# Kernel tuning notes

Measured on AMD Instinct MI355X. Metric: run time of the kernel, lower is better.

Reference implementation:

```python
import jax, jax.numpy as jnp
import numpy as np

N = 50000   # nodes
E = 600000  # edges per relation
F = 256     # dim_features
H = 128     # dim_hiddens == dim_embs
Q = 64      # dim_query
R = 2       # relations per sign (etypes)
L = 2       # conv_depth


def setup_inputs() -> dict:
    key = jax.random.key(0)
    ks = jax.random.split(key, 11)
    s = 0.05
    return {
        "x_attr": jax.random.normal(ks[0], (N, F), jnp.float32),
        "x_stru": jax.random.normal(ks[1], (N, F), jnp.float32),
        # edges_*: [sign(pos/neg), relation, (src,dst), E]
        "edges_attr": jax.random.randint(ks[2], (2, R, 2, E), 0, N),
        "edges_stru": jax.random.randint(ks[3], (2, R, 2, E), 0, N),
        # params, leading dim 2 = (pos_emb_model, neg_emb_model)
        "Wf": jax.random.normal(ks[4], (2, H, F), jnp.float32) * s,
        "convW": jax.random.normal(ks[5], (2, L, R, H, H), jnp.float32) * s,
        "convB": jnp.zeros((2, L, R, H), jnp.float32),
        "attnW1": jax.random.normal(ks[6], (2, L, H, Q), jnp.float32) * s,
        "attnB1": jnp.zeros((2, L, Q), jnp.float32),
        "attnW2": jax.random.normal(ks[7], (2, L, Q), jnp.float32) * s,
        "Wc": jax.random.normal(ks[8], (2, H, 3 * H), jnp.float32) * s,
    }


def _gcn(h, src, dst, W, b):
    """DGL GraphConv, norm='both', degrees clamped to >=1."""
    n = h.shape[0]
    ones = jnp.ones(src.shape[0], h.dtype)
    deg_out = jnp.clip(jax.ops.segment_sum(ones, src, num_segments=n), 1.0)
    deg_in = jnp.clip(jax.ops.segment_sum(ones, dst, num_segments=n), 1.0)
    m = (h * (deg_out ** -0.5)[:, None]) @ W          # (N, H)
    agg = jax.ops.segment_sum(m[src], dst, num_segments=n)  # gather-scatter over edges
    return agg * (deg_in ** -0.5)[:, None] + b


def _het_layer(h, edges, Ws, bs, W1, b1, w2):
    """HeteroGraphConv with per-node attention aggregation over relations.
    edges: (R, 2, E); Ws: (R,H,H); bs: (R,H)."""
    hs = jnp.stack([_gcn(h, edges[r, 0], edges[r, 1], Ws[r], bs[r]) for r in range(R)])  # (R,N,H)
    scores = jnp.einsum('rnq,q->rn', jnp.tanh(jnp.einsum('rnd,dq->rnq', hs, W1) + b1), w2)
    a = jax.nn.softmax(scores, axis=0)                # (R,N) attention over relations
    return jnp.einsum('rn,rnd->nd', a, hs), a


def _hetattn(x, edges, Wf, cW, cB, aW1, aB1, aW2, Wc):
    h0 = jnp.tanh(x @ Wf.T)                                        # (N,H)
    h1, _ = _het_layer(h0, edges, cW[1], cB[1], aW1[1], aB1[1], aW2[1])   # 1-hop via last conv
    hA, _ = _het_layer(h0, edges, cW[0], cB[0], aW1[0], aB1[0], aW2[0])
    h2, attn = _het_layer(hA, edges, cW[1], cB[1], aW1[1], aB1[1], aW2[1])  # 2-hop
    y = jnp.concatenate([h0, h1, h2], axis=-1) @ Wc.T              # concat_weight
    return y, attn.T


def reference(x_attr, x_stru, edges_attr, edges_stru, Wf, convW, convB,
              attnW1, attnB1, attnW2, Wc):
    def run(sign, x, edges):
        y, _ = _hetattn(x, edges[sign], Wf[sign], convW[sign], convB[sign],
                        attnW1[sign], attnB1[sign], attnW2[sign], Wc[sign])
        return y
    embs_attr_pos = run(0, x_attr, edges_attr)
    embs_stru_pos = run(0, x_stru, edges_stru)
    embs_attr_neg = run(1, x_attr, edges_attr)
    embs_stru_neg = run(1, x_stru, edges_stru)
    return (embs_attr_pos, embs_stru_pos, embs_attr_neg, embs_stru_neg)
```

## Files before the change

### kernel.cpp

```cpp
#include <hip/hip_runtime.h>
#include <math.h>

constexpr int N_ = 50000;
constexpr int E_ = 600000;
constexpr int F_ = 256;
constexpr int H_ = 128;
constexpr int Q_ = 64;
constexpr int R_ = 2;
constexpr int L_ = 2;

#define MODE_STORE 0
#define MODE_TANH  1
#define MODE_ACC   2

template <bool BT>
__global__ __launch_bounds__(256) void gemm_kernel(
    const float* __restrict__ A, int lda,
    const float* __restrict__ B, int ldb,
    float* __restrict__ C, int ldc,
    int M, int K,
    const float* __restrict__ rowscale, int mode)
{
    __shared__ __align__(16) float As[2][16][68];
    __shared__ __align__(16) float Bs[2][16][132];

    const int row0 = blockIdx.x * 64;
    const int col0 = blockIdx.y * 128;
    const int tid  = threadIdx.x;
    const int tm = tid >> 4;
    const int tn = tid & 15;

    const int am  = tid >> 2;
    const int ak4 = (tid & 3) * 4;
    const int bj  = tid >> 1;
    const int bk8 = (tid & 1) * 8;
    const int bk  = tid >> 5;
    const int bj4 = (tid & 31) * 4;

    auto loadA = [&](int kk) -> float4 {
        const int r = row0 + am;
        if (r < M) return *(const float4*)(A + (size_t)r * lda + kk + ak4);
        return make_float4(0.f, 0.f, 0.f, 0.f);
    };
    auto loadB = [&](int kk, float4& v0, float4& v1) {
        if (BT) {
            const float* bp = B + (size_t)(col0 + bj) * ldb + kk + bk8;
            v0 = *(const float4*)(bp);
            v1 = *(const float4*)(bp + 4);
        } else {
            v0 = *(const float4*)(B + (size_t)(kk + bk) * ldb + col0 + bj4);
            v1 = *(const float4*)(B + (size_t)(kk + bk + 8) * ldb + col0 + bj4);
        }
    };
    auto storeT = [&](int b, float4 va, float4 v0, float4 v1) {
        As[b][ak4 + 0][am] = va.x; As[b][ak4 + 1][am] = va.y;
        As[b][ak4 + 2][am] = va.z; As[b][ak4 + 3][am] = va.w;
        if (BT) {
            Bs[b][bk8 + 0][bj] = v0.x; Bs[b][bk8 + 1][bj] = v0.y;
            Bs[b][bk8 + 2][bj] = v0.z; Bs[b][bk8 + 3][bj] = v0.w;
            Bs[b][bk8 + 4][bj] = v1.x; Bs[b][bk8 + 5][bj] = v1.y;
            Bs[b][bk8 + 6][bj] = v1.z; Bs[b][bk8 + 7][bj] = v1.w;
        } else {
            Bs[b][bk + 0][bj4 + 0] = v0.x; Bs[b][bk + 0][bj4 + 1] = v0.y;
            Bs[b][bk + 0][bj4 + 2] = v0.z; Bs[b][bk + 0][bj4 + 3] = v0.w;
            Bs[b][bk + 8][bj4 + 0] = v1.x; Bs[b][bk + 8][bj4 + 1] = v1.y;
            Bs[b][bk + 8][bj4 + 2] = v1.z; Bs[b][bk + 8][bj4 + 3] = v1.w;
        }
    };

    float acc[4][8] = {};

    {
        float4 va = loadA(0), v0, v1;
        loadB(0, v0, v1);
        storeT(0, va, v0, v1);
    }
    __syncthreads();

    int cur = 0;
    for (int kk = 16; ; kk += 16) {
        const bool more = (kk < K);
        float4 na, n0, n1;
        if (more) { na = loadA(kk); loadB(kk, n0, n1); }

        #pragma unroll
        for (int k = 0; k < 16; k++) {
            const float4 av  = *(const float4*)&As[cur][k][tm * 4];
            const float4 bv0 = *(const float4*)&Bs[cur][k][tn * 8];
            const float4 bv1 = *(const float4*)&Bs[cur][k][tn * 8 + 4];
            const float a[4] = {av.x, av.y, av.z, av.w};
            const float b[8] = {bv0.x, bv0.y, bv0.z, bv0.w,
                                bv1.x, bv1.y, bv1.z, bv1.w};
            #pragma unroll
            for (int i = 0; i < 4; i++)
                #pragma unroll
                for (int j = 0; j < 8; j++)
                    acc[i][j] += a[i] * b[j];
        }
        if (!more) break;
        storeT(cur ^ 1, na, n0, n1);
        __syncthreads();
        cur ^= 1;
    }

    #pragma unroll
    for (int i = 0; i < 4; i++) {
        const int r = row0 + tm * 4 + i;
        if (r >= M) continue;
        const float rs = rowscale ? rowscale[r] : 1.0f;
        #pragma unroll
        for (int j = 0; j < 8; j++) {
            const int c = col0 + tn * 8 + j;
            float v = acc[i][j] * rs;
            if (mode == MODE_TANH) v = tanhf(v);
            float* p = C + (size_t)r * ldc + c;
            if (mode == MODE_ACC) *p += v;
            else                  *p = v;
        }
    }
}

__global__ __launch_bounds__(256) void gemm_conv_pair(
    const float* __restrict__ A, int lda,
    const float* __restrict__ B0, const float* __restrict__ B1,
    float* __restrict__ C0, float* __restrict__ C1,
    int M, const float* __restrict__ rs0, const float* __restrict__ rs1)
{
    __shared__ __align__(16) float As[2][16][68];
    __shared__ __align__(16) float B0s[2][16][68];
    __shared__ __align__(16) float B1s[2][16][68];

    const int row0 = blockIdx.x * 64;
    const int col0 = blockIdx.y * 64;
    const int tid  = threadIdx.x;
    const int tm = tid >> 4;
    const int tn = tid & 15;

    const int am  = tid >> 2;
    const int ak4 = (tid & 3) * 4;
    const int bk  = tid >> 4;
    const int bj4 = (tid & 15) * 4;

    auto loadA = [&](int kk) -> float4 {
        const int r = row0 + am;
        if (r < M) return *(const float4*)(A + (size_t)r * lda + kk + ak4);
        return make_float4(0.f, 0.f, 0.f, 0.f);
    };
    auto storeT = [&](int b, float4 va, float4 v0, float4 v1) {
        As[b][ak4 + 0][am] = va.x; As[b][ak4 + 1][am] = va.y;
        As[b][ak4 + 2][am] = va.z; As[b][ak4 + 3][am] = va.w;
        B0s[b][bk][bj4 + 0] = v0.x; B0s[b][bk][bj4 + 1] = v0.y;
        B0s[b][bk][bj4 + 2] = v0.z; B0s[b][bk][bj4 + 3] = v0.w;
        B1s[b][bk][bj4 + 0] = v1.x; B1s[b][bk][bj4 + 1] = v1.y;
        B1s[b][bk][bj4 + 2] = v1.z; B1s[b][bk][bj4 + 3] = v1.w;
    };

    float acc0[4][4] = {};
    float acc1[4][4] = {};

    {
        float4 va = loadA(0);
        float4 v0 = *(const float4*)(B0 + (size_t)bk * H_ + col0 + bj4);
        float4 v1 = *(const float4*)(B1 + (size_t)bk * H_ + col0 + bj4);
        storeT(0, va, v0, v1);
    }
    __syncthreads();

    int cur = 0;
    for (int kk = 16; ; kk += 16) {
        const bool more = (kk < H_);
        float4 na, n0, n1;
        if (more) {
            na = loadA(kk);
            n0 = *(const float4*)(B0 + (size_t)(kk + bk) * H_ + col0 + bj4);
            n1 = *(const float4*)(B1 + (size_t)(kk + bk) * H_ + col0 + bj4);
        }

        #pragma unroll
        for (int k = 0; k < 16; k++) {
            const float4 av  = *(const float4*)&As[cur][k][tm * 4];
            const float4 bv0 = *(const float4*)&B0s[cur][k][tn * 4];
            const float4 bv1 = *(const float4*)&B1s[cur][k][tn * 4];
            const float a[4]  = {av.x, av.y, av.z, av.w};
            const float b0[4] = {bv0.x, bv0.y, bv0.z, bv0.w};
            const float b1v[4] = {bv1.x, bv1.y, bv1.z, bv1.w};
            #pragma unroll
            for (int i = 0; i < 4; i++)
                #pragma unroll
                for (int j = 0; j < 4; j++) {
                    acc0[i][j] += a[i] * b0[j];
                    acc1[i][j] += a[i] * b1v[j];
                }
        }
        if (!more) break;
        storeT(cur ^ 1, na, n0, n1);
        __syncthreads();
        cur ^= 1;
    }

    #pragma unroll
    for (int i = 0; i < 4; i++) {
        const int r = row0 + tm * 4 + i;
        if (r >= M) continue;
        const float s0 = rs0[r];
        const float s1 = rs1[r];
        #pragma unroll
        for (int j = 0; j < 4; j++) {
            const int c = col0 + tn * 4 + j;
            C0[(size_t)r * H_ + c] = acc0[i][j] * s0;
            C1[(size_t)r * H_ + c] = acc1[i][j] * s1;
        }
    }
}

__global__ __launch_bounds__(256) void zero_i(int* __restrict__ p, int n)
{
    int t = blockIdx.x * 256 + threadIdx.x;
    if (t < n) p[t] = 0;
}

__global__ __launch_bounds__(256) void count_deg(const int* __restrict__ eb,
                                                 int* __restrict__ cnt, int total)
{
    int t = blockIdx.x * 256 + threadIdx.x;
    if (t >= total) return;
    int which = t / E_;
    atomicAdd(&cnt[which * N_ + eb[t]], 1);
}

__global__ __launch_bounds__(256) void deg_finalize(const int* __restrict__ cnt,
                                                    float* __restrict__ dscale, int n)
{
    int t = blockIdx.x * 256 + threadIdx.x;
    if (t < n) {
        int v = cnt[t];
        dscale[t] = rsqrtf((float)(v < 1 ? 1 : v));
    }
}

constexpr int SCAN_NB = (N_ + 255) / 256;

__global__ __launch_bounds__(256) void scan_p1(const int* __restrict__ cnt,
                                               int* __restrict__ bsums)
{
    const int r = blockIdx.y;
    const int* in = cnt + (size_t)(2 * r + 1) * N_;
    const int i = blockIdx.x * 256 + threadIdx.x;
    int v = (i < N_) ? in[i] : 0;
    #pragma unroll
    for (int off = 32; off > 0; off >>= 1) v += __shfl_xor(v, off);
    __shared__ int ws[4];
    if ((threadIdx.x & 63) == 0) ws[threadIdx.x >> 6] = v;
    __syncthreads();
    if (threadIdx.x == 0)
        bsums[r * SCAN_NB + blockIdx.x] = ws[0] + ws[1] + ws[2] + ws[3];
}

__global__ __launch_bounds__(256) void scan_p2(int* __restrict__ bsums)
{
    __shared__ int sh[256];
    const int r = blockIdx.x;
    const int t = threadIdx.x;
    int v = (t < SCAN_NB) ? bsums[r * SCAN_NB + t] : 0;
    sh[t] = v;
    __syncthreads();
    #pragma unroll
    for (int d = 1; d < 256; d <<= 1) {
        int u = (t >= d) ? sh[t - d] : 0;
        __syncthreads();
        sh[t] += u;
        __syncthreads();
    }
    if (t < SCAN_NB) bsums[r * SCAN_NB + t] = sh[t] - v;
}

__global__ __launch_bounds__(256) void scan_p3(const int* __restrict__ cnt,
                                               const int* __restrict__ bsums,
                                               int* __restrict__ offs,
                                               int* __restrict__ cursor)
{
    __shared__ int sh[256];
    const int r = blockIdx.y;
    const int* in = cnt + (size_t)(2 * r + 1) * N_;
    int* out = offs + (size_t)r * (N_ + 1);
    int* cur = cursor + (size_t)r * N_;
    const int i = blockIdx.x * 256 + threadIdx.x;
    const int t = threadIdx.x;
    int v = (i < N_) ? in[i] : 0;
    sh[t] = v;
    __syncthreads();
    #pragma unroll
    for (int d = 1; d < 256; d <<= 1) {
        int u = (t >= d) ? sh[t - d] : 0;
        __syncthreads();
        sh[t] += u;
        __syncthreads();
    }
    const int excl = sh[t] - v + bsums[r * SCAN_NB + blockIdx.x];
    if (i < N_) { out[i] = excl; cur[i] = excl; }
    if (i == 0) out[N_] = E_;
}

__global__ __launch_bounds__(256) void csr_fill(const int* __restrict__ eb,
                                                int* __restrict__ cursor,
                                                int* __restrict__ csr, int total)
{
    int t = blockIdx.x * 256 + threadIdx.x;
    if (t >= total) return;
    int r = (t >= E_) ? 1 : 0;
    int e = t - r * E_;
    int s = eb[(r * 2 + 0) * E_ + e];
    int d = eb[(r * 2 + 1) * E_ + e];
    int pos = atomicAdd(&cursor[r * N_ + d], 1);
    csr[(size_t)r * E_ + pos] = s;
}

__device__ __forceinline__ void gather_rel(const float2* __restrict__ m,
                                           const int* __restrict__ csr,
                                           int b, int e, int lane, float2& acc)
{
    int k = b;
    for (; k + 4 <= e; k += 4) {
        const int s0 = csr[k + 0];
        const int s1 = csr[k + 1];
        const int s2 = csr[k + 2];
        const int s3 = csr[k + 3];
        const float2 v0 = m[(size_t)s0 * 64 + lane];
        const float2 v1 = m[(size_t)s1 * 64 + lane];
        const float2 v2 = m[(size_t)s2 * 64 + lane];
        const float2 v3 = m[(size_t)s3 * 64 + lane];
        acc.x += (v0.x + v1.x) + (v2.x + v3.x);
        acc.y += (v0.y + v1.y) + (v2.y + v3.y);
    }
    for (; k < e; k++) {
        const int s = csr[k];
        const float2 v = m[(size_t)s * 64 + lane];
        acc.x += v.x; acc.y += v.y;
    }
}

__global__ __launch_bounds__(1024, 8) void pull_attn(
    const float2* __restrict__ m0, const float2* __restrict__ m1,
    const int* __restrict__ offs0, const int* __restrict__ csr0,
    const int* __restrict__ offs1, const int* __restrict__ csr1,
    const float* __restrict__ si0, const float* __restrict__ si1,
    const float* __restrict__ bias0, const float* __restrict__ bias1,
    const float* __restrict__ W1, const float* __restrict__ b1,
    const float* __restrict__ w2, float2* __restrict__ outb, int n)
{
    __shared__ float W1s[H_ * Q_];
    __shared__ __align__(16) float2 hsS[16][2][Q_];
    __shared__ float b1s[Q_], w2s[Q_], bAs[H_], bBs[H_];

    for (int i = threadIdx.x; i < H_ * Q_; i += 1024) W1s[i] = W1[i];
    if (threadIdx.x < Q_) { b1s[threadIdx.x] = b1[threadIdx.x]; w2s[threadIdx.x] = w2[threadIdx.x]; }
    {
        const int t = (int)threadIdx.x - Q_;
        if (t >= 0 && t < H_) bAs[t] = bias0[t];
        const int u = (int)threadIdx.x - Q_ - H_;
        if (u >= 0 && u < H_) bBs[u] = bias1[u];
    }
    __syncthreads();

    const int lane = threadIdx.x & 63;
    const int wv   = threadIdx.x >> 6;
    int node = (blockIdx.x * 1024 + threadIdx.x) >> 6;
    node = __builtin_amdgcn_readfirstlane(node);

    float2 hs0 = make_float2(0.f, 0.f), hs1 = hs0;

    if (node < n) {
        float2 a0 = make_float2(0.f, 0.f), a1 = a0;
        const int b0  = offs0[node], e0 = offs0[node + 1];
        const int b1i = offs1[node], e1 = offs1[node + 1];
        gather_rel(m0, csr0, b0,  e0, lane, a0);
        gather_rel(m1, csr1, b1i, e1, lane, a1);

        const float sc0 = si0[node], sc1 = si1[node];
        hs0.x = a0.x * sc0 + bAs[2 * lane];
        hs0.y = a0.y * sc0 + bAs[2 * lane + 1];
        hs1.x = a1.x * sc1 + bBs[2 * lane];
        hs1.y = a1.y * sc1 + bBs[2 * lane + 1];
        hsS[wv][0][lane] = hs0;
        hsS[wv][1][lane] = hs1;
    }

    __asm__ volatile("s_waitcnt lgkmcnt(0)" ::: "memory");
    __builtin_amdgcn_sched_barrier(0);

    if (node < n) {
        const float4* h0p4 = (const float4*)&hsS[wv][0][0];
        const float4* h1p4 = (const float4*)&hsS[wv][1][0];
        float t0 = b1s[lane], t1 = b1s[lane];
        #pragma unroll 8
        for (int i4 = 0; i4 < 32; i4++) {
            const float4 h0v = h0p4[i4];
            const float4 h1v = h1p4[i4];
            const float wa = W1s[(i4 * 4 + 0) * Q_ + lane];
            const float wb = W1s[(i4 * 4 + 1) * Q_ + lane];
            const float wc = W1s[(i4 * 4 + 2) * Q_ + lane];
            const float wd = W1s[(i4 * 4 + 3) * Q_ + lane];
            t0 += h0v.x * wa + h0v.y * wb + h0v.z * wc + h0v.w * wd;
            t1 += h1v.x * wa + h1v.y * wb + h1v.z * wc + h1v.w * wd;
        }
        float s0 = tanhf(t0) * w2s[lane];
        float s1 = tanhf(t1) * w2s[lane];
        #pragma unroll
        for (int off = 32; off > 0; off >>= 1) {
            s0 += __shfl_xor(s0, off);
            s1 += __shfl_xor(s1, off);
        }
        const float mx = fmaxf(s0, s1);
        const float e0v = expf(s0 - mx), e1v = expf(s1 - mx);
        const float a0 = e0v / (e0v + e1v), a1 = 1.0f - a0;

        float2 o;
        o.x = a0 * hs0.x + a1 * hs1.x;
        o.y = a0 * hs0.y + a1 * hs1.y;
        outb[(size_t)node * 64 + lane] = o;
    }
}

extern "C" void kernel_launch(void* const* d_in, const int* in_sizes, int n_in,
                              void* d_out, int out_size, void* d_ws, size_t ws_size,
                              hipStream_t stream)
{
    const float* x_attr = (const float*)d_in[0];
    const float* x_stru = (const float*)d_in[1];
    const int*   e_attr = (const int*)d_in[2];
    const int*   e_stru = (const int*)d_in[3];
    const float* Wf     = (const float*)d_in[4];
    const float* convW  = (const float*)d_in[5];
    const float* convB  = (const float*)d_in[6];
    const float* aW1    = (const float*)d_in[7];
    const float* aB1    = (const float*)d_in[8];
    const float* aW2    = (const float*)d_in[9];
    const float* Wc     = (const float*)d_in[10];
    float*       out    = (float*)d_out;
    float*       ws     = (float*)d_ws;

    const size_t NH = (size_t)N_ * H_;
    float* A  = ws;
    float* Bb = ws + 1 * NH;
    float* C  = ws + 2 * NH;
    float* D  = ws + 3 * NH;
    float* dscale = ws + 4 * NH;
    int*   ibase  = (int*)(dscale + 4 * N_);
    int*   cnt    = ibase;
    int*   offs   = ibase + 4 * N_;
    int*   csr    = offs + 2 * (N_ + 1);
    int*   cursor = csr + 2 * E_;
    int*   bsums  = cursor + 2 * N_;

    const int GX = (N_ + 63) / 64;
    const dim3 GGEMM(GX, 1);
    const dim3 GCONV(GX, 2);
    const dim3 GSCAN(SCAN_NB, 2);
    const int PA_B = (N_ * 64) / 1024;

    for (int run = 0; run < 4; run++) {
        const int sign = run >> 1;
        const float* x = (run & 1) ? x_stru : x_attr;
        const int* eb = ((run & 1) ? e_stru : e_attr) + (size_t)sign * (R_ * 2 * E_);
        float* y = out + (size_t)run * NH;
        const float* WcS = Wc + (size_t)sign * H_ * 3 * H_;

        zero_i<<<(4 * N_ + 255) / 256, 256, 0, stream>>>(cnt, 4 * N_);
        count_deg<<<(4 * E_ + 255) / 256, 256, 0, stream>>>(eb, cnt, 4 * E_);
        deg_finalize<<<(4 * N_ + 255) / 256, 256, 0, stream>>>(cnt, dscale, 4 * N_);
        scan_p1<<<GSCAN, 256, 0, stream>>>(cnt, bsums);
        scan_p2<<<2, 256, 0, stream>>>(bsums);
        scan_p3<<<GSCAN, 256, 0, stream>>>(cnt, bsums, offs, cursor);
        csr_fill<<<(2 * E_ + 255) / 256, 256, 0, stream>>>(eb, cursor, csr, 2 * E_);

        gemm_kernel<true><<<GGEMM, 256, 0, stream>>>(
            x, F_, Wf + (size_t)sign * H_ * F_, F_, A, H_, N_, F_, nullptr, MODE_TANH);

        gemm_kernel<true><<<GGEMM, 256, 0, stream>>>(
            A, H_, WcS, 3 * H_, y, H_, N_, H_, nullptr, MODE_STORE);

        auto het = [&](const float* h_in, int l, float* outb) {
            const size_t lo = (size_t)(sign * L_ + l);
            gemm_conv_pair<<<GCONV, 256, 0, stream>>>(
                h_in, H_,
                convW + (lo * R_ + 0) * H_ * H_,
                convW + (lo * R_ + 1) * H_ * H_,
                C, D, N_,
                dscale + 0 * N_, dscale + 2 * N_);
            pull_attn<<<PA_B, 1024, 0, stream>>>(
                (const float2*)C, (const float2*)D,
                offs, csr, offs + (N_ + 1), csr + E_,
                dscale + N_, dscale + 3 * N_,
                convB + (lo * R_ + 0) * H_, convB + (lo * R_ + 1) * H_,
                aW1 + lo * H_ * Q_, aB1 + lo * Q_, aW2 + lo * Q_,
                (float2*)outb, N_);
        };

        het(A, 1, Bb);
        gemm_kernel<true><<<GGEMM, 256, 0, stream>>>(
            Bb, H_, WcS + H_, 3 * H_, y, H_, N_, H_, nullptr, MODE_ACC);

        het(A, 0, Bb);

        het(Bb, 1, A);
        gemm_kernel<true><<<GGEMM, 256, 0, stream>>>(
            A, H_, WcS + 2 * H_, 3 * H_, y, H_, N_, H_, nullptr, MODE_ACC);
    }
}
```

Baseline: 3.467 ms.

## Aggregate before transform, share first-hop gather, fold attention projection into conv GEMM

Each layer now gathers neighbours first and then applies the GEMM, instead of transforming first and then gathering. The per-edge source-degree scale is stored alongside the CSR during construction. Because the 1-hop pass and layer 0 both aggregate h0, they share one gather, so each run does two gathers instead of three. The attention projection W·W1 and its bias are precomputed once, so the conv GEMM emits both the hidden output and the attention pre-activations, and a light kernel applies tanh, softmax and the combine. The cost is an extra buffer for the scores, per-edge scale reads in the gather, and a wider GEMM tile.

```diff
diff --git a/kernel.cpp b/kernel.cpp
--- a/kernel.cpp
+++ b/kernel.cpp
@@ -120,96 +120,142 @@
     }
 }
 
-__global__ __launch_bounds__(256) void gemm_conv_pair(
-    const float* __restrict__ A, int lda,
-    const float* __restrict__ B0, const float* __restrict__ B1,
-    float* __restrict__ C0, float* __restrict__ C1,
-    int M, const float* __restrict__ rs0, const float* __restrict__ rs1)
+__global__ __launch_bounds__(256) void conv_dual(
+    const float* g0, const float* g1,
+    const float* __restrict__ Wlo,
+    const float* __restrict__ WWlo,
+    float* hs0, float* hs1,
+    float* T,
+    int M)
 {
     __shared__ __align__(16) float As[2][16][68];
-    __shared__ __align__(16) float B0s[2][16][68];
-    __shared__ __align__(16) float B1s[2][16][68];
+    __shared__ __align__(16) float Bs[2][16][200];
+
+    const int r = blockIdx.y;
+    const float* A  = r ? g1 : g0;
+    const float* __restrict__ W  = Wlo  + (size_t)r * H_ * H_;
+    const float* __restrict__ WW = WWlo + (size_t)r * H_ * Q_;
+    float* hs = r ? hs1 : hs0;
+    float* Tr = T + (size_t)r * M * Q_;
 
     const int row0 = blockIdx.x * 64;
-    const int col0 = blockIdx.y * 64;
     const int tid  = threadIdx.x;
     const int tm = tid >> 4;
     const int tn = tid & 15;
 
     const int am  = tid >> 2;
     const int ak4 = (tid & 3) * 4;
-    const int bk  = tid >> 4;
-    const int bj4 = (tid & 15) * 4;
+
+    int bk_[3], bc_[3];
+    #pragma unroll
+    for (int i = 0; i < 3; i++) {
+        const int f = tid + i * 256;
+        bk_[i] = f / 48;
+        bc_[i] = (f % 48) * 4;
+    }
 
     auto loadA = [&](int kk) -> float4 {
-        const int r = row0 + am;
-        if (r < M) return *(const float4*)(A + (size_t)r * lda + kk + ak4);
+        const int rr = row0 + am;
+        if (rr < M) return *(const float4*)(A + (size_t)rr * H_ + kk + ak4);
         return make_float4(0.f, 0.f, 0.f, 0.f);
     };
-    auto storeT = [&](int b, float4 va, float4 v0, float4 v1) {
+    auto loadB = [&](int kk, float4* v) {
+        #pragma unroll
+        for (int i = 0; i < 3; i++) {
+            const int k = kk + bk_[i];
+            const int c = bc_[i];
+            v[i] = (c < H_) ? *(const float4*)(W  + (size_t)k * H_ + c)
+                            : *(const float4*)(WW + (size_t)k * Q_ + (c - H_));
+        }
+    };
+    auto storeT = [&](int b, float4 va, const float4* v) {
         As[b][ak4 + 0][am] = va.x; As[b][ak4 + 1][am] = va.y;
         As[b][ak4 + 2][am] = va.z; As[b][ak4 + 3][am] = va.w;
-        B0s[b][bk][bj4 + 0] = v0.x; B0s[b][bk][bj4 + 1] = v0.y;
-        B0s[b][bk][bj4 + 2] = v0.z; B0s[b][bk][bj4 + 3] = v0.w;
-        B1s[b][bk][bj4 + 0] = v1.x; B1s[b][bk][bj4 + 1] = v1.y;
-        B1s[b][bk][bj4 + 2] = v1.z; B1s[b][bk][bj4 + 3] = v1.w;
+        #pragma unroll
+        for (int i = 0; i < 3; i++) {
+            Bs[b][bk_[i]][bc_[i] + 0] = v[i].x;
+            Bs[b][bk_[i]][bc_[i] + 1] = v[i].y;
+            Bs[b][bk_[i]][bc_[i] + 2] = v[i].z;
+            Bs[b][bk_[i]][bc_[i] + 3] = v[i].w;
+        }
     };
 
-    float acc0[4][4] = {};
-    float acc1[4][4] = {};
+    float acc[4][12] = {};
 
     {
-        float4 va = loadA(0);
-        float4 v0 = *(const float4*)(B0 + (size_t)bk * H_ + col0 + bj4);
-        float4 v1 = *(const float4*)(B1 + (size_t)bk * H_ + col0 + bj4);
-        storeT(0, va, v0, v1);
+        float4 va = loadA(0), vb[3];
+        loadB(0, vb);
+        storeT(0, va, vb);
     }
     __syncthreads();
 
     int cur = 0;
     for (int kk = 16; ; kk += 16) {
         const bool more = (kk < H_);
-        float4 na, n0, n1;
-        if (more) {
-            na = loadA(kk);
-            n0 = *(const float4*)(B0 + (size_t)(kk + bk) * H_ + col0 + bj4);
-            n1 = *(const float4*)(B1 + (size_t)(kk + bk) * H_ + col0 + bj4);
-        }
+        float4 na, nb[3];
+        if (more) { na = loadA(kk); loadB(kk, nb); }
 
         #pragma unroll
         for (int k = 0; k < 16; k++) {
             const float4 av  = *(const float4*)&As[cur][k][tm * 4];
-            const float4 bv0 = *(const float4*)&B0s[cur][k][tn * 4];
-            const float4 bv1 = *(const float4*)&B1s[cur][k][tn * 4];
+            const float4 bv0 = *(const float4*)&Bs[cur][k][tn * 12];
+            const float4 bv1 = *(const float4*)&Bs[cur][k][tn * 12 + 4];
+            const float4 bv2 = *(const float4*)&Bs[cur][k][tn * 12 + 8];
             const float a[4]  = {av.x, av.y, av.z, av.w};
-            const float b0[4] = {bv0.x, bv0.y, bv0.z, bv0.w};
-            const float b1v[4] = {bv1.x, bv1.y, bv1.z, bv1.w};
+            const float b[12] = {bv0.x, bv0.y, bv0.z, bv0.w,
+                                 bv1.x, bv1.y, bv1.z, bv1.w,
+                                 bv2.x, bv2.y, bv2.z, bv2.w};
             #pragma unroll
             for (int i = 0; i < 4; i++)
                 #pragma unroll
-                for (int j = 0; j < 4; j++) {
-                    acc0[i][j] += a[i] * b0[j];
-                    acc1[i][j] += a[i] * b1v[j];
-                }
+                for (int j = 0; j < 12; j++)
+                    acc[i][j] += a[i] * b[j];
         }
         if (!more) break;
-        storeT(cur ^ 1, na, n0, n1);
+        storeT(cur ^ 1, na, nb);
         __syncthreads();
         cur ^= 1;
     }
 
     #pragma unroll
     for (int i = 0; i < 4; i++) {
-        const int r = row0 + tm * 4 + i;
-        if (r >= M) continue;
-        const float s0 = rs0[r];
-        const float s1 = rs1[r];
+        const int rr = row0 + tm * 4 + i;
+        if (rr >= M) continue;
         #pragma unroll
-        for (int j = 0; j < 4; j++) {
-            const int c = col0 + tn * 4 + j;
-            C0[(size_t)r * H_ + c] = acc0[i][j] * s0;
-            C1[(size_t)r * H_ + c] = acc1[i][j] * s1;
-        }
+        for (int j = 0; j < 12; j++) {
+            const int c = tn * 12 + j;
+            const float v = acc[i][j];
+            if (c < H_) hs[(size_t)rr * H_ + c] = v;
+            else        Tr[(size_t)rr * Q_ + (c - H_)] = v;
+        }
+    }
+}
+
+__global__ __launch_bounds__(256) void prep_ww1(
+    const float* __restrict__ convW, const float* __restrict__ convB,
+    const float* __restrict__ aW1, const float* __restrict__ aB1,
+    float* __restrict__ ww1, float* __restrict__ bbq)
+{
+    const int c  = blockIdx.x;
+    const int lo = c >> 1;
+    const int r  = c & 1;
+    const float* W  = convW + ((size_t)lo * R_ + r) * H_ * H_;
+    const float* W1 = aW1 + (size_t)lo * H_ * Q_;
+    const float* bs = convB + ((size_t)lo * R_ + r) * H_;
+    const float* b1 = aB1 + (size_t)lo * Q_;
+    float* o = ww1 + (size_t)c * H_ * Q_;
+
+    for (int ofs = threadIdx.x; ofs < H_ * Q_; ofs += 256) {
+        const int k = ofs >> 6, q = ofs & 63;
+        float s = 0.f;
+        for (int i = 0; i < H_; i++) s += W[k * H_ + i] * W1[i * Q_ + q];
+        o[ofs] = s;
+    }
+    if (threadIdx.x < Q_) {
+        const int q = threadIdx.x;
+        float s = 0.f;
+        for (int i = 0; i < H_; i++) s += bs[i] * W1[i * Q_ + q];
+        bbq[c * Q_ + q] = s + b1[q];
     }
 }
 
@@ -303,7 +349,9 @@
 
 __global__ __launch_bounds__(256) void csr_fill(const int* __restrict__ eb,
                                                 int* __restrict__ cursor,
-                                                int* __restrict__ csr, int total)
+                                                int* __restrict__ csr,
+                                                const float* __restrict__ dscale,
+                                                float* __restrict__ scl, int total)
 {
     int t = blockIdx.x * 256 + threadIdx.x;
     if (t >= total) return;
@@ -313,112 +361,112 @@
     int d = eb[(r * 2 + 1) * E_ + e];
     int pos = atomicAdd(&cursor[r * N_ + d], 1);
     csr[(size_t)r * E_ + pos] = s;
-}
-
-__device__ __forceinline__ void gather_rel(const float2* __restrict__ m,
-                                           const int* __restrict__ csr,
-                                           int b, int e, int lane, float2& acc)
-{
-    int k = b;
-    for (; k + 4 <= e; k += 4) {
-        const int s0 = csr[k + 0];
-        const int s1 = csr[k + 1];
-        const int s2 = csr[k + 2];
-        const int s3 = csr[k + 3];
-        const float2 v0 = m[(size_t)s0 * 64 + lane];
-        const float2 v1 = m[(size_t)s1 * 64 + lane];
-        const float2 v2 = m[(size_t)s2 * 64 + lane];
-        const float2 v3 = m[(size_t)s3 * 64 + lane];
-        acc.x += (v0.x + v1.x) + (v2.x + v3.x);
-        acc.y += (v0.y + v1.y) + (v2.y + v3.y);
-    }
-    for (; k < e; k++) {
-        const int s = csr[k];
-        const float2 v = m[(size_t)s * 64 + lane];
-        acc.x += v.x; acc.y += v.y;
-    }
-}
-
-__global__ __launch_bounds__(1024, 8) void pull_attn(
-    const float2* __restrict__ m0, const float2* __restrict__ m1,
-    const int* __restrict__ offs0, const int* __restrict__ csr0,
-    const int* __restrict__ offs1, const int* __restrict__ csr1,
+    scl[(size_t)r * E_ + pos] = dscale[(size_t)(2 * r) * N_ + s];
+}
+
+__global__ __launch_bounds__(256) void gather2(
+    const float2* __restrict__ h,
+    const int* __restrict__ offs0, const int* __restrict__ csr0, const float* __restrict__ scl0,
+    const int* __restrict__ offs1, const int* __restrict__ csr1, const float* __restrict__ scl1,
+    float2* __restrict__ g0, float2* __restrict__ g1, int n)
+{
+    const int lane = threadIdx.x & 63;
+    int node = (blockIdx.x * 256 + threadIdx.x) >> 6;
+    node = __builtin_amdgcn_readfirstlane(node);
+    if (node >= n) return;
+
+    float2 a0 = make_float2(0.f, 0.f), a1 = a0;
+    {
+        int k = offs0[node];
+        const int e = offs0[node + 1];
+        for (; k + 4 <= e; k += 4) {
+            const int s0 = csr0[k + 0], s1 = csr0[k + 1];
+            const int s2 = csr0[k + 2], s3 = csr0[k + 3];
+            const float w0 = scl0[k + 0], w1 = scl0[k + 1];
+            const float w2v = scl0[k + 2], w3 = scl0[k + 3];
+            const float2 v0 = h[(size_t)s0 * 64 + lane];
+            const float2 v1 = h[(size_t)s1 * 64 + lane];
+            const float2 v2 = h[(size_t)s2 * 64 + lane];
+            const float2 v3 = h[(size_t)s3 * 64 + lane];
+            a0.x += v0.x * w0 + v1.x * w1 + v2.x * w2v + v3.x * w3;
+            a0.y += v0.y * w0 + v1.y * w1 + v2.y * w2v + v3.y * w3;
+        }
+        for (; k < e; k++) {
+            const int s = csr0[k];
+            const float w = scl0[k];
+            const float2 v = h[(size_t)s * 64 + lane];
+            a0.x += v.x * w; a0.y += v.y * w;
+        }
+    }
+    {
+        int k = offs1[node];
+        const int e = offs1[node + 1];
+        for (; k + 4 <= e; k += 4) {
+            const int s0 = csr1[k + 0], s1 = csr1[k + 1];
+            const int s2 = csr1[k + 2], s3 = csr1[k + 3];
+            const float w0 = scl1[k + 0], w1 = scl1[k + 1];
+            const float w2v = scl1[k + 2], w3 = scl1[k + 3];
+            const float2 v0 = h[(size_t)s0 * 64 + lane];
+            const float2 v1 = h[(size_t)s1 * 64 + lane];
+            const float2 v2 = h[(size_t)s2 * 64 + lane];
+            const float2 v3 = h[(size_t)s3 * 64 + lane];
+            a1.x += v0.x * w0 + v1.x * w1 + v2.x * w2v + v3.x * w3;
+            a1.y += v0.y * w0 + v1.y * w1 + v2.y * w2v + v3.y * w3;
+        }
+        for (; k < e; k++) {
+            const int s = csr1[k];
+            const float w = scl1[k];
+            const float2 v = h[(size_t)s * 64 + lane];
+            a1.x += v.x * w; a1.y += v.y * w;
+        }
+    }
+    g0[(size_t)node * 64 + lane] = a0;
+    g1[(size_t)node * 64 + lane] = a1;
+}
+
+__global__ __launch_bounds__(256) void attn_comb(
+    const float2* hs0p, const float2* hs1p,
+    const float* __restrict__ T0, const float* __restrict__ T1,
     const float* __restrict__ si0, const float* __restrict__ si1,
     const float* __restrict__ bias0, const float* __restrict__ bias1,
-    const float* __restrict__ W1, const float* __restrict__ b1,
-    const float* __restrict__ w2, float2* __restrict__ outb, int n)
-{
-    __shared__ float W1s[H_ * Q_];
-    __shared__ __align__(16) float2 hsS[16][2][Q_];
-    __shared__ float b1s[Q_], w2s[Q_], bAs[H_], bBs[H_];
-
-    for (int i = threadIdx.x; i < H_ * Q_; i += 1024) W1s[i] = W1[i];
-    if (threadIdx.x < Q_) { b1s[threadIdx.x] = b1[threadIdx.x]; w2s[threadIdx.x] = w2[threadIdx.x]; }
-    {
-        const int t = (int)threadIdx.x - Q_;
-        if (t >= 0 && t < H_) bAs[t] = bias0[t];
-        const int u = (int)threadIdx.x - Q_ - H_;
-        if (u >= 0 && u < H_) bBs[u] = bias1[u];
-    }
+    const float* __restrict__ bbq0, const float* __restrict__ bbq1,
+    const float* __restrict__ w2,
+    float2* outb, int n)
+{
+    __shared__ float bbqA[Q_], bbqB[Q_], w2s[Q_], bAs[H_], bBs[H_];
+    const int tid = threadIdx.x;
+    if (tid < Q_) { bbqA[tid] = bbq0[tid]; w2s[tid] = w2[tid]; }
+    else if (tid < 2 * Q_) bbqB[tid - Q_] = bbq1[tid - Q_];
+    if (tid < H_) bAs[tid] = bias0[tid];
+    else bBs[tid - H_] = bias1[tid - H_];
     __syncthreads();
 
-    const int lane = threadIdx.x & 63;
-    const int wv   = threadIdx.x >> 6;
-    int node = (blockIdx.x * 1024 + threadIdx.x) >> 6;
+    const int lane = tid & 63;
+    int node = (blockIdx.x * 256 + tid) >> 6;
     node = __builtin_amdgcn_readfirstlane(node);
-
-    float2 hs0 = make_float2(0.f, 0.f), hs1 = hs0;
-
-    if (node < n) {
-        float2 a0 = make_float2(0.f, 0.f), a1 = a0;
-        const int b0  = offs0[node], e0 = offs0[node + 1];
-        const int b1i = offs1[node], e1 = offs1[node + 1];
-        gather_rel(m0, csr0, b0,  e0, lane, a0);
-        gather_rel(m1, csr1, b1i, e1, lane, a1);
-
-        const float sc0 = si0[node], sc1 = si1[node];
-        hs0.x = a0.x * sc0 + bAs[2 * lane];
-        hs0.y = a0.y * sc0 + bAs[2 * lane + 1];
-        hs1.x = a1.x * sc1 + bBs[2 * lane];
-        hs1.y = a1.y * sc1 + bBs[2 * lane + 1];
-        hsS[wv][0][lane] = hs0;
-        hsS[wv][1][lane] = hs1;
-    }
-
-    __asm__ volatile("s_waitcnt lgkmcnt(0)" ::: "memory");
-    __builtin_amdgcn_sched_barrier(0);
-
-    if (node < n) {
-        const float4* h0p4 = (const float4*)&hsS[wv][0][0];
-        const float4* h1p4 = (const float4*)&hsS[wv][1][0];
-        float t0 = b1s[lane], t1 = b1s[lane];
-        #pragma unroll 8
-        for (int i4 = 0; i4 < 32; i4++) {
-            const float4 h0v = h0p4[i4];
-            const float4 h1v = h1p4[i4];
-            const float wa = W1s[(i4 * 4 + 0) * Q_ + lane];
-            const float wb = W1s[(i4 * 4 + 1) * Q_ + lane];
-            const float wc = W1s[(i4 * 4 + 2) * Q_ + lane];
-            const float wd = W1s[(i4 * 4 + 3) * Q_ + lane];
-            t0 += h0v.x * wa + h0v.y * wb + h0v.z * wc + h0v.w * wd;
-            t1 += h1v.x * wa + h1v.y * wb + h1v.z * wc + h1v.w * wd;
-        }
-        float s0 = tanhf(t0) * w2s[lane];
-        float s1 = tanhf(t1) * w2s[lane];
-        #pragma unroll
-        for (int off = 32; off > 0; off >>= 1) {
-            s0 += __shfl_xor(s0, off);
-            s1 += __shfl_xor(s1, off);
-        }
-        const float mx = fmaxf(s0, s1);
-        const float e0v = expf(s0 - mx), e1v = expf(s1 - mx);
-        const float a0 = e0v / (e0v + e1v), a1 = 1.0f - a0;
-
-        float2 o;
-        o.x = a0 * hs0.x + a1 * hs1.x;
-        o.y = a0 * hs0.y + a1 * hs1.y;
-        outb[(size_t)node * 64 + lane] = o;
-    }
+    if (node >= n) return;
+
+    const float t0v = T0[(size_t)node * Q_ + lane];
+    const float t1v = T1[(size_t)node * Q_ + lane];
+    const float si0n = si0[node], si1n = si1[node];
+    const float2 h0v = hs0p[(size_t)node * 64 + lane];
+    const float2 h1v = hs1p[(size_t)node * 64 + lane];
+
+    float s0 = tanhf(si0n * t0v + bbqA[lane]) * w2s[lane];
+    float s1 = tanhf(si1n * t1v + bbqB[lane]) * w2s[lane];
+    #pragma unroll
+    for (int off = 32; off > 0; off >>= 1) {
+        s0 += __shfl_xor(s0, off);
+        s1 += __shfl_xor(s1, off);
+    }
+    const float mx = fmaxf(s0, s1);
+    const float e0v = expf(s0 - mx), e1v = expf(s1 - mx);
+    const float a0 = e0v / (e0v + e1v), a1 = 1.0f - a0;
+
+    float2 o;
+    o.x = a0 * (h0v.x * si0n + bAs[2 * lane])     + a1 * (h1v.x * si1n + bBs[2 * lane]);
+    o.y = a0 * (h0v.y * si0n + bAs[2 * lane + 1]) + a1 * (h1v.y * si1n + bBs[2 * lane + 1]);
+    outb[(size_t)node * 64 + lane] = o;
 }
 
 extern "C" void kernel_launch(void* const* d_in, const int* in_sizes, int n_in,
@@ -444,19 +492,26 @@
     float* Bb = ws + 1 * NH;
     float* C  = ws + 2 * NH;
     float* D  = ws + 3 * NH;
-    float* dscale = ws + 4 * NH;
+    float* Tb = ws + 4 * NH;
+    float* dscale = ws + 5 * NH;
     int*   ibase  = (int*)(dscale + 4 * N_);
     int*   cnt    = ibase;
-    int*   offs   = ibase + 4 * N_;
-    int*   csr    = offs + 2 * (N_ + 1);
+    int*   offs   = cnt + 4 * N_;
+    constexpr int OFFS_PAD = 2 * (N_ + 1) + 2;
+    int*   csr    = offs + OFFS_PAD;
     int*   cursor = csr + 2 * E_;
     int*   bsums  = cursor + 2 * N_;
+    float* scl    = (float*)(bsums + 2 * SCAN_NB);
+    float* ww1    = scl + 2 * (size_t)E_;
+    float* bbq    = ww1 + 8 * H_ * Q_;
 
     const int GX = (N_ + 63) / 64;
     const dim3 GGEMM(GX, 1);
     const dim3 GCONV(GX, 2);
     const dim3 GSCAN(SCAN_NB, 2);
-    const int PA_B = (N_ * 64) / 1024;
+    const int PW_B = (N_ * 64) / 256;
+
+    prep_ww1<<<8, 256, 0, stream>>>(convW, convB, aW1, aB1, ww1, bbq);
 
     for (int run = 0; run < 4; run++) {
         const int sign = run >> 1;
@@ -471,7 +526,8 @@
         scan_p1<<<GSCAN, 256, 0, stream>>>(cnt, bsums);
         scan_p2<<<2, 256, 0, stream>>>(bsums);
         scan_p3<<<GSCAN, 256, 0, stream>>>(cnt, bsums, offs, cursor);
-        csr_fill<<<(2 * E_ + 255) / 256, 256, 0, stream>>>(eb, cursor, csr, 2 * E_);
+        csr_fill<<<(2 * E_ + 255) / 256, 256, 0, stream>>>(eb, cursor, csr,
+                                                           dscale, scl, 2 * E_);
 
         gemm_kernel<true><<<GGEMM, 256, 0, stream>>>(
             x, F_, Wf + (size_t)sign * H_ * F_, F_, A, H_, N_, F_, nullptr, MODE_TANH);
@@ -479,31 +535,39 @@
         gemm_kernel<true><<<GGEMM, 256, 0, stream>>>(
             A, H_, WcS, 3 * H_, y, H_, N_, H_, nullptr, MODE_STORE);
 
-        auto het = [&](const float* h_in, int l, float* outb) {
+        gather2<<<PW_B, 256, 0, stream>>>(
+            (const float2*)A, offs, csr, scl, offs + (N_ + 1), csr + E_, scl + E_,
+            (float2*)C, (float2*)D, N_);
+
+        auto convattn = [&](int l, float* hsA, float* hsB, float* dest) {
             const size_t lo = (size_t)(sign * L_ + l);
-            gemm_conv_pair<<<GCONV, 256, 0, stream>>>(
-                h_in, H_,
-                convW + (lo * R_ + 0) * H_ * H_,
-                convW + (lo * R_ + 1) * H_ * H_,
-                C, D, N_,
-                dscale + 0 * N_, dscale + 2 * N_);
-            pull_attn<<<PA_B, 1024, 0, stream>>>(
-                (const float2*)C, (const float2*)D,
-                offs, csr, offs + (N_ + 1), csr + E_,
+            conv_dual<<<GCONV, 256, 0, stream>>>(
+                C, D,
+                convW + lo * R_ * H_ * H_,
+                ww1 + lo * R_ * H_ * Q_,
+                hsA, hsB, Tb, N_);
+            attn_comb<<<PW_B, 256, 0, stream>>>(
+                (const float2*)hsA, (const float2*)hsB,
+                Tb, Tb + (size_t)N_ * Q_,
                 dscale + N_, dscale + 3 * N_,
                 convB + (lo * R_ + 0) * H_, convB + (lo * R_ + 1) * H_,
-                aW1 + lo * H_ * Q_, aB1 + lo * Q_, aW2 + lo * Q_,
-                (float2*)outb, N_);
+                bbq + (lo * 2 + 0) * Q_, bbq + (lo * 2 + 1) * Q_,
+                aW2 + lo * Q_,
+                (float2*)dest, N_);
         };
 
-        het(A, 1, Bb);
+        convattn(1, A, Bb, Bb);
         gemm_kernel<true><<<GGEMM, 256, 0, stream>>>(
             Bb, H_, WcS + H_, 3 * H_, y, H_, N_, H_, nullptr, MODE_ACC);
 
-        het(A, 0, Bb);
-
-        het(Bb, 1, A);
+        convattn(0, C, D, A);
+
+        gather2<<<PW_B, 256, 0, stream>>>(
+            (const float2*)A, offs, csr, scl, offs + (N_ + 1), csr + E_, scl + E_,
+            (float2*)C, (float2*)D, N_);
+
+        convattn(1, C, D, C);
         gemm_kernel<true><<<GGEMM, 256, 0, stream>>>(
-            A, H_, WcS + 2 * H_, 3 * H_, y, H_, N_, H_, nullptr, MODE_ACC);
-    }
-}
+            C, H_, WcS + 2 * H_, 3 * H_, y, H_, N_, H_, nullptr, MODE_ACC);
+    }
+}
```

Measured after the change: 4.185 ms. +20.7%, slower.
